# Kernel tuning notes

Measured on AMD Instinct MI355X. Metric: run time of the kernel, lower is better.

Reference implementation:

```python
import jax, jax.numpy as jnp
import numpy as np

B, S, D_MODEL, D_K, D_V = 8, 2048, 1024, 64, 64
NEG = -1e9


def setup_inputs() -> dict:
    key = jax.random.key(0)
    ks = jax.random.split(key, 12)
    inv = 1.0 / np.sqrt(D_MODEL)
    return {
        "q": jax.random.normal(ks[0], (B, S, D_MODEL), jnp.float32),
        "k": jax.random.normal(ks[1], (B, S, D_MODEL), jnp.float32),
        "v": jax.random.normal(ks[2], (B, S, D_MODEL), jnp.float32),
        "mask": jax.random.randint(ks[3], (1, S, S), 0, 2, jnp.int32),
        # Linear weights stored as [in, out] so y = x @ W + b
        "Wq": jax.random.normal(ks[4], (D_MODEL, D_K), jnp.float32) * inv,
        "bq": jnp.zeros((D_K,), jnp.float32),
        "Wk": jax.random.normal(ks[5], (D_MODEL, D_K), jnp.float32) * inv,
        "bk": jnp.zeros((D_K,), jnp.float32),
        "Wv": jax.random.normal(ks[6], (D_MODEL, D_V), jnp.float32) * inv,
        "bv": jnp.zeros((D_V,), jnp.float32),
        "Wo": jax.random.normal(ks[7], (D_V, D_MODEL), jnp.float32) * (1.0 / np.sqrt(D_V)),
        "bo": jnp.zeros((D_MODEL,), jnp.float32),
    }


def reference(q, k, v, mask, Wq, bq, Wk, bk, Wv, bv, Wo, bo):
    # single-head projections: [b, s, d_model] -> [b, s, d_k/d_v]
    qp = q @ Wq + bq
    kp = k @ Wk + bk
    vp = v @ Wv + bv
    # UNSCALED dot-product scores (original has no 1/sqrt(d_k)): [b, s, s]
    scores = jnp.einsum("bqd,bkd->bqk", qp, kp)
    scores = jnp.where(mask == 0, jnp.float32(NEG), scores)
    attn = jax.nn.softmax(scores, axis=-1)  # dropout p=0.0 -> identity
    out = jnp.einsum("bqk,bkv->bqv", attn, vp)
    return out @ Wo + bo
```

## Files before the change

### kernel.cpp

```cpp
#include <hip/hip_runtime.h>
#include <hip/hip_bf16.h>

typedef __bf16 bf16_t;
typedef __attribute__((ext_vector_type(8))) __bf16 bf16x8;
typedef __attribute__((ext_vector_type(4))) float f32x4;

#define MFMA16(a, b, c) __builtin_amdgcn_mfma_f32_16x16x32_bf16((a), (b), (c), 0, 0, 0)

#define NB 8
#define SS 2048
#define DM 1024
#define DK 64
#define NROW (NB * SS)
#define NSPLIT 4
#define SPLEN (SS / NSPLIT)

typedef __attribute__((address_space(1))) const unsigned int ga_u32;
typedef __attribute__((address_space(3))) unsigned int ls_u32;
#define GLOAD16(g, l) \
  __builtin_amdgcn_global_load_lds((ga_u32*)(g), (ls_u32*)(l), 16, 0, 0)

union U16x8 { unsigned short u[8]; uint4 q; };
union U16x4 { unsigned short u[4]; ushort4 v; };

__device__ inline void split_hl(float x, unsigned short& h, unsigned short& l) {
  bf16_t hb = (bf16_t)x;
  bf16_t lb = (bf16_t)(x - (float)hb);
  h = *(unsigned short*)&hb;
  l = *(unsigned short*)&lb;
}

__global__ __launch_bounds__(256) void maskpack_kernel(
    const int* __restrict__ mask, unsigned int* __restrict__ mbits) {
  int idx = blockIdx.x * 256 + threadIdx.x;
  int q = idx >> 6, w = idx & 63;
  const int4* src = (const int4*)(mask + (q << 11) + (w << 5));
  unsigned int bits = 0u;
#pragma unroll
  for (int i = 0; i < 8; ++i) {
    int4 t = src[i];
    bits |= (t.x != 0 ? 1u : 0u) << (i * 4 + 0);
    bits |= (t.y != 0 ? 1u : 0u) << (i * 4 + 1);
    bits |= (t.z != 0 ? 1u : 0u) << (i * 4 + 2);
    bits |= (t.w != 0 ? 1u : 0u) << (i * 4 + 3);
  }
  mbits[idx] = bits;
}

__global__ __launch_bounds__(256) void wprep_kernel(
    const float* __restrict__ Wq, const float* __restrict__ Wk,
    const float* __restrict__ Wv, char* __restrict__ wimg) {
  int which = blockIdx.x >> 6;
  const float* W = which == 0 ? Wq : (which == 1 ? Wk : Wv);
  char* img = wimg + (size_t)which * 16 * 16384;
  int e = (blockIdx.x & 63) * 256 + threadIdx.x;
  int k = e >> 4, n0 = (e & 15) << 2;
  float4 f = *(const float4*)(W + k * 64 + n0);
  float fv[4] = {f.x, f.y, f.z, f.w};
  char* base = img + (k >> 6) * 16384;
  int kk = k & 63;
#pragma unroll
  for (int u = 0; u < 4; ++u) {
    int n = n0 + u;
    unsigned short h, l;
    split_hl(fv[u], h, l);
    int byte = n * 128 + ((2 * kk) ^ ((n & 7) << 4));
    *(unsigned short*)(base + byte) = h;
    *(unsigned short*)(base + 8192 + byte) = l;
  }
}

__global__ __launch_bounds__(256) void proj3_kernel(
    const float* __restrict__ qx, const float* __restrict__ kx,
    const float* __restrict__ vx, const char* __restrict__ wimg,
    const float* __restrict__ bq, const float* __restrict__ bk,
    const float* __restrict__ bv, bf16_t* __restrict__ qhi,
    bf16_t* __restrict__ qlo, char* __restrict__ kimg,
    char* __restrict__ vimg) {
  __shared__ __align__(16) char smem[49664];
  char* xbuf = smem;
  char* wbuf = smem + 33280;
  const int mode = blockIdx.y;
  const float* X = mode == 0 ? qx : (mode == 1 ? kx : vx);
  const float* bias = mode == 0 ? bq : (mode == 1 ? bk : bv);
  const char* Xb = (const char*)X;
  const int tid = threadIdx.x;
  const int lane = tid & 63;
  const int wv = tid >> 6;
  const int lr = lane & 15;
  const int g = lane >> 4;
  const int wm = wv & 1;
  const int wn = wv >> 1;
  const int rbase = blockIdx.x * 32;
  const char* wsrc0 = wimg + (size_t)mode * 16 * 16384;

  f32x4 acc[2] = {};

  auto stageX = [&](int sc) {
#pragma unroll
    for (int j = 0; j < 8; ++j) {
      int u = wv * 8 + j;
      GLOAD16(Xb + (size_t)(rbase + u) * 4096 + sc * 1024 + lane * 16,
              xbuf + u * 1040 + lane * 16);
    }
  };
  auto stageW = [&](int idx) {
    const char* wsrc = wsrc0 + idx * 16384;
#pragma unroll
    for (int v = 0; v < 4; ++v)
      GLOAD16(wsrc + v * 4096 + tid * 16, wbuf + v * 4096 + tid * 16);
  };

  stageX(0);
  stageW(0);
  asm volatile("s_waitcnt vmcnt(0)" ::: "memory");
  __builtin_amdgcn_s_barrier();
  __builtin_amdgcn_sched_barrier(0);

  for (int idx = 0; idx < 16; ++idx) {
    {
      const int sub = idx & 3;
      const char* xrow = xbuf + (wm * 16 + lr) * 1040 + sub * 256;
#pragma unroll
      for (int ks = 0; ks < 2; ++ks) {
        float4 f0 = *(const float4*)(xrow + ks * 128 + g * 32);
        float4 f1 = *(const float4*)(xrow + ks * 128 + g * 32 + 16);
        float xv[8] = {f0.x, f0.y, f0.z, f0.w, f1.x, f1.y, f1.z, f1.w};
        bf16x8 ah, al;
#pragma unroll
        for (int i = 0; i < 8; ++i) {
          unsigned short h, l;
          split_hl(xv[i], h, l);
          ((unsigned short*)&ah)[i] = h;
          ((unsigned short*)&al)[i] = l;
        }
#pragma unroll
        for (int c = 0; c < 2; ++c) {
          int n = wn * 32 + c * 16 + lr;
          int swb = (n & 7) << 4;
          int co = ks * 64 + g * 16;
          bf16x8 bh = *(const bf16x8*)(wbuf + n * 128 + (co ^ swb));
          bf16x8 bl = *(const bf16x8*)(wbuf + 8192 + n * 128 + (co ^ swb));
          acc[c] = MFMA16(ah, bl, acc[c]);
          acc[c] = MFMA16(al, bh, acc[c]);
          acc[c] = MFMA16(ah, bh, acc[c]);
        }
      }
    }
    __builtin_amdgcn_sched_barrier(0);
    __builtin_amdgcn_s_barrier();
    if (idx < 15) {
      if ((idx & 3) == 3) stageX((idx >> 2) + 1);
      stageW(idx + 1);
      asm volatile("s_waitcnt vmcnt(0)" ::: "memory");
      __builtin_amdgcn_s_barrier();
      __builtin_amdgcn_sched_barrier(0);
    }
  }

  __syncthreads();
  float* sacc = (float*)smem;
#pragma unroll
  for (int c = 0; c < 2; ++c)
#pragma unroll
    for (int j = 0; j < 4; ++j)
      sacc[(wm * 16 + g * 4 + j) * 69 + wn * 32 + c * 16 + lr] = acc[c][j];
  __syncthreads();

  const int b = rbase >> 11;
  const int t = (rbase & (SS - 1)) >> 6;
  const int rt0 = rbase & 63;
  if (mode == 0) {
    int r = tid & 31, cg = tid >> 5;
    int row = rbase + r;
    U16x8 h, l;
#pragma unroll
    for (int i = 0; i < 8; ++i) {
      float v = sacc[r * 69 + cg * 8 + i] + bias[cg * 8 + i];
      split_hl(v, h.u[i], l.u[i]);
    }
    *(uint4*)((char*)qhi + (size_t)row * 128 + cg * 16) = h.q;
    *(uint4*)((char*)qlo + (size_t)row * 128 + cg * 16) = l.q;
  } else if (mode == 1) {
    int r = tid & 31, cg = tid >> 5;
    int rr = rt0 + r;
    char* base = kimg + (((size_t)(b * 32 + t)) << 14);
    int off = rr * 128 + ((cg * 16) ^ ((rr & 7) << 4));
    U16x8 h, l;
#pragma unroll
    for (int i = 0; i < 8; ++i) {
      float v = sacc[r * 69 + cg * 8 + i] + bias[cg * 8 + i];
      split_hl(v, h.u[i], l.u[i]);
    }
    *(uint4*)(base + off) = h.q;
    *(uint4*)(base + 8192 + off) = l.q;
  } else {
    int d = tid & 63, rg = tid >> 6;
    char* base = vimg + (((size_t)(b * 32 + t)) << 14);
    float bv = bias[d];
    U16x8 h, l;
#pragma unroll
    for (int i = 0; i < 8; ++i) {
      float v = sacc[(rg * 8 + i) * 69 + d] + bv;
      split_hl(v, h.u[i], l.u[i]);
    }
    int off = d * 128 + (((rt0 + rg * 8) * 2) ^ ((d & 7) << 4));
    *(uint4*)(base + off) = h.q;
    *(uint4*)(base + 8192 + off) = l.q;
  }
}

__global__ __launch_bounds__(256) void attn_kernel(
    const bf16_t* __restrict__ qhi, const bf16_t* __restrict__ qlo,
    const char* __restrict__ kimg, const char* __restrict__ vimg,
    const unsigned int* __restrict__ mbits, float* __restrict__ part_acc,
    float* __restrict__ part_m, float* __restrict__ part_l) {
  __shared__ __align__(16) char kbuf[16384];
  __shared__ __align__(16) char vbuf[16384];
  __shared__ __align__(16) char plds_all[4][2048];
  const int tid = threadIdx.x;
  const int lane = tid & 63;
  const int wv = tid >> 6;
  const int lr = lane & 15;
  const int g = lane >> 4;
  char* plds = &plds_all[wv][0];
  const int qrow0 = (blockIdx.x * 4 + wv) * 16;
  const int split = blockIdx.y;
  const int kv0 = split * SPLEN;
  const int b = qrow0 >> 11;
  const int sq0 = (qrow0 & (SS - 1)) + g * 4;

  const bf16_t* qh = qhi + (qrow0 + lr) * DK + g * 8;
  const bf16_t* ql = qlo + (qrow0 + lr) * DK + g * 8;
  bf16x8 qh0 = *(const bf16x8*)qh;
  bf16x8 qh1 = *(const bf16x8*)(qh + 32);
  bf16x8 ql0 = *(const bf16x8*)ql;
  bf16x8 ql1 = *(const bf16x8*)(ql + 32);

  float m[4], lsum[4];
  f32x4 acc[4] = {};
#pragma unroll
  for (int j = 0; j < 4; ++j) { m[j] = -3.0e38f; lsum[j] = 0.f; }

  for (int it = 0; it < SPLEN / 64; ++it) {
    const int tglob = (kv0 >> 6) + it;
    const char* ksrc = kimg + (((size_t)(b * 32 + tglob)) << 14);
    const char* vsrc = vimg + (((size_t)(b * 32 + tglob)) << 14);
#pragma unroll
    for (int u = 0; u < 4; ++u) {
      GLOAD16(ksrc + tid * 16 + u * 4096, kbuf + tid * 16 + u * 4096);
      GLOAD16(vsrc + tid * 16 + u * 4096, vbuf + tid * 16 + u * 4096);
    }
    asm volatile("s_waitcnt vmcnt(0)\n" ::: "memory");
    __syncthreads();
    f32x4 sac[4];
#pragma unroll
    for (int t = 0; t < 4; ++t) {
      int rk = t * 16 + lr;
      int sw = (rk & 7) << 4;
      bf16x8 kh0 = *(const bf16x8*)(kbuf + rk * 128 + ((g * 16) ^ sw));
      bf16x8 kh1 = *(const bf16x8*)(kbuf + rk * 128 + ((64 + g * 16) ^ sw));
      bf16x8 kl0 = *(const bf16x8*)(kbuf + 8192 + rk * 128 + ((g * 16) ^ sw));
      bf16x8 kl1 =
          *(const bf16x8*)(kbuf + 8192 + rk * 128 + ((64 + g * 16) ^ sw));
      f32x4 s = {};
      s = MFMA16(qh0, kl0, s);
      s = MFMA16(qh1, kl1, s);
      s = MFMA16(ql0, kh0, s);
      s = MFMA16(ql1, kh1, s);
      s = MFMA16(qh0, kh0, s);
      s = MFMA16(qh1, kh1, s);
      sac[t] = s;
    }
    const int wbase = (kv0 >> 5) + it * 2;
    uint2 m2[4];
#pragma unroll
    for (int j = 0; j < 4; ++j)
      m2[j] = *(const uint2*)(mbits + (sq0 + j) * 64 + wbase);
#pragma unroll
    for (int t = 0; t < 4; ++t)
#pragma unroll
      for (int j = 0; j < 4; ++j) {
        unsigned w = (t & 2) ? m2[j].y : m2[j].x;
        if (!((w >> ((t & 1) * 16 + lr)) & 1u)) sac[t][j] = -1e9f;
      }
#pragma unroll
    for (int j = 0; j < 4; ++j) {
      float v = sac[0][j];
#pragma unroll
      for (int t = 1; t < 4; ++t) v = fmaxf(v, sac[t][j]);
      v = fmaxf(v, __shfl_xor(v, 1, 64));
      v = fmaxf(v, __shfl_xor(v, 2, 64));
      v = fmaxf(v, __shfl_xor(v, 4, 64));
      v = fmaxf(v, __shfl_xor(v, 8, 64));
      float mn = fmaxf(m[j], v);
      float sc = __expf(m[j] - mn);
      m[j] = mn;
      lsum[j] *= sc;
#pragma unroll
      for (int c = 0; c < 4; ++c) acc[c][j] *= sc;
    }
    float ps[4] = {0.f, 0.f, 0.f, 0.f};
#pragma unroll
    for (int t = 0; t < 4; ++t)
#pragma unroll
      for (int j = 0; j < 4; ++j) {
        float p = __expf(sac[t][j] - m[j]);
        bf16_t pb = (bf16_t)p;
        ps[j] += (float)pb;
        int row = g * 4 + j;
        int byte = row * 128 + (((t * 16 + lr) * 2) ^ ((row & 7) << 4));
        *(bf16_t*)(plds + byte) = pb;
      }
#pragma unroll
    for (int j = 0; j < 4; ++j) {
      float s_ = ps[j];
      s_ += __shfl_xor(s_, 1, 64);
      s_ += __shfl_xor(s_, 2, 64);
      s_ += __shfl_xor(s_, 4, 64);
      s_ += __shfl_xor(s_, 8, 64);
      lsum[j] += s_;
    }
    asm volatile("s_waitcnt lgkmcnt(0)\n" ::: "memory");
#pragma unroll
    for (int kt = 0; kt < 2; ++kt) {
      int pbyte = lr * 128 + ((kt * 64 + g * 16) ^ ((lr & 7) << 4));
      bf16x8 pa = *(const bf16x8*)(plds + pbyte);
#pragma unroll
      for (int c = 0; c < 4; ++c) {
        int n = c * 16 + lr;
        int swv = (n & 7) << 4;
        bf16x8 vfh = *(const bf16x8*)(vbuf + n * 128 + ((kt * 64 + g * 16) ^ swv));
        bf16x8 vfl =
            *(const bf16x8*)(vbuf + 8192 + n * 128 + ((kt * 64 + g * 16) ^ swv));
        acc[c] = MFMA16(pa, vfh, acc[c]);
        acc[c] = MFMA16(pa, vfl, acc[c]);
      }
    }
    __syncthreads();
  }
#pragma unroll
  for (int c = 0; c < 4; ++c)
#pragma unroll
    for (int j = 0; j < 4; ++j)
      part_acc[((size_t)split * NROW + qrow0 + g * 4 + j) * DK + c * 16 + lr] =
          acc[c][j];
  if (lr == 0) {
#pragma unroll
    for (int j = 0; j < 4; ++j) {
      part_m[split * NROW + qrow0 + g * 4 + j] = m[j];
      part_l[split * NROW + qrow0 + g * 4 + j] = lsum[j];
    }
  }
}

__global__ __launch_bounds__(256) void combine_kernel(
    const float* __restrict__ pacc, const float* __restrict__ pm,
    const float* __restrict__ pl, float* __restrict__ attn_f) {
  int idx = blockIdx.x * 256 + threadIdx.x;
  int row = idx >> 6;
  float m0 = pm[row], m1 = pm[NROW + row];
  float m2 = pm[2 * NROW + row], m3 = pm[3 * NROW + row];
  float M = fmaxf(fmaxf(m0, m1), fmaxf(m2, m3));
  float w0 = __expf(m0 - M), w1 = __expf(m1 - M);
  float w2 = __expf(m2 - M), w3 = __expf(m3 - M);
  float l = w0 * pl[row] + w1 * pl[NROW + row] + w2 * pl[2 * NROW + row] +
            w3 * pl[3 * NROW + row];
  float a = w0 * pacc[idx] + w1 * pacc[(size_t)NROW * DK + idx] +
            w2 * pacc[2 * (size_t)NROW * DK + idx] +
            w3 * pacc[3 * (size_t)NROW * DK + idx];
  attn_f[idx] = a / l;
}

__global__ __launch_bounds__(256) void oproj_kernel(
    const float* __restrict__ attn, const float* __restrict__ Wo,
    const float* __restrict__ bo, float* __restrict__ out) {
  __shared__ __align__(16) bf16_t wt[256 * 64];
  const int tid = threadIdx.x;
  const int lane = tid & 63;
  const int wv = tid >> 6;
  const int lr = lane & 15;
  const int g = lane >> 4;
  const int rbase = blockIdx.x * 64 + wv * 16;
  const int c0 = blockIdx.y * 256;
  {
    const int k = tid >> 2;
    const int n0 = (tid & 3) << 6;
    const float4* src = (const float4*)(Wo + k * DM + c0 + n0);
#pragma unroll
    for (int i = 0; i < 16; ++i) {
      float4 f = src[i];
      float fv[4] = {f.x, f.y, f.z, f.w};
#pragma unroll
      for (int u = 0; u < 4; ++u) {
        int n = n0 + i * 4 + u;
        int byte = (n << 7) + (k << 1);
        byte ^= (n & 7) << 4;
        *(bf16_t*)((char*)wt + byte) = (bf16_t)fv[u];
      }
    }
  }
  __syncthreads();
  const float* ab = attn + (rbase + lr) * DK + g * 8;
  float4 x0 = *(const float4*)ab;
  float4 x1 = *(const float4*)(ab + 4);
  float4 y0 = *(const float4*)(ab + 32);
  float4 y1 = *(const float4*)(ab + 36);
  float xv[8] = {x0.x, x0.y, x0.z, x0.w, x1.x, x1.y, x1.z, x1.w};
  float yv[8] = {y0.x, y0.y, y0.z, y0.w, y1.x, y1.y, y1.z, y1.w};
  bf16x8 ah0, al0, ah1, al1;
#pragma unroll
  for (int i = 0; i < 8; ++i) {
    ah0[i] = (bf16_t)xv[i];
    al0[i] = (bf16_t)(xv[i] - (float)ah0[i]);
    ah1[i] = (bf16_t)yv[i];
    al1[i] = (bf16_t)(yv[i] - (float)ah1[i]);
  }
  f32x4 acc[16] = {};
#pragma unroll
  for (int c = 0; c < 16; ++c) {
    int n = c * 16 + lr;
    int byte0 = (n << 7) + ((g * 8) << 1);
    byte0 ^= (n & 7) << 4;
    int byte1 = (n << 7) + ((32 + g * 8) << 1);
    byte1 ^= (n & 7) << 4;
    bf16x8 b0 = *(const bf16x8*)((const char*)wt + byte0);
    bf16x8 b1 = *(const bf16x8*)((const char*)wt + byte1);
    acc[c] = MFMA16(ah0, b0, acc[c]);
    acc[c] = MFMA16(al0, b0, acc[c]);
    acc[c] = MFMA16(ah1, b1, acc[c]);
    acc[c] = MFMA16(al1, b1, acc[c]);
  }
#pragma unroll
  for (int c = 0; c < 16; ++c) {
    float bv = bo[c0 + c * 16 + lr];
#pragma unroll
    for (int j = 0; j < 4; ++j)
      out[(rbase + g * 4 + j) * DM + c0 + c * 16 + lr] = acc[c][j] + bv;
  }
}

extern "C" void kernel_launch(void* const* d_in, const int* in_sizes, int n_in,
                              void* d_out, int out_size, void* d_ws,
                              size_t ws_size, hipStream_t stream) {
  const float* q = (const float*)d_in[0];
  const float* k = (const float*)d_in[1];
  const float* v = (const float*)d_in[2];
  const int* mask = (const int*)d_in[3];
  const float* Wq = (const float*)d_in[4];
  const float* bq = (const float*)d_in[5];
  const float* Wk = (const float*)d_in[6];
  const float* bk = (const float*)d_in[7];
  const float* Wv = (const float*)d_in[8];
  const float* bv = (const float*)d_in[9];
  const float* Wo = (const float*)d_in[10];
  const float* bo = (const float*)d_in[11];
  float* out = (float*)d_out;

  bf16_t* qhi = (bf16_t*)d_ws;
  bf16_t* qlo = qhi + (size_t)NROW * DK;
  char* kimg = (char*)(qlo + (size_t)NROW * DK);
  char* vimg = kimg + ((size_t)NB * 32 << 14);
  char* wimg = vimg + ((size_t)NB * 32 << 14);
  float* part_acc = (float*)(wimg + (size_t)3 * 16 * 16384);
  float* part_m = part_acc + (size_t)NSPLIT * NROW * DK;
  float* part_l = part_m + (size_t)NSPLIT * NROW;
  float* attn_f = part_l + (size_t)NSPLIT * NROW;
  unsigned int* mbits = (unsigned int*)(attn_f + (size_t)NROW * DK);

  maskpack_kernel<<<dim3(SS * (SS / 32) / 256), dim3(256), 0, stream>>>(mask,
                                                                        mbits);
  wprep_kernel<<<dim3(192), dim3(256), 0, stream>>>(Wq, Wk, Wv, wimg);
  proj3_kernel<<<dim3(NROW / 32, 3), dim3(256), 0, stream>>>(
      q, k, v, wimg, bq, bk, bv, qhi, qlo, kimg, vimg);
  attn_kernel<<<dim3(NROW / 64, NSPLIT), dim3(256), 0, stream>>>(
      qhi, qlo, kimg, vimg, mbits, part_acc, part_m, part_l);
  combine_kernel<<<dim3(NROW * DK / 256), dim3(256), 0, stream>>>(
      part_acc, part_m, part_l, attn_f);
  oproj_kernel<<<dim3(NROW / 64, DM / 256), dim3(256), 0, stream>>>(attn_f, Wo,
                                                                    bo, out);
}
```

Before: 147.7 us.

## Double-buffer weight tiles and prefetch X through registers with split-once bf16 conversion

```diff
diff --git a/kernel.cpp b/kernel.cpp
--- a/kernel.cpp
+++ b/kernel.cpp
@@ -77,13 +77,11 @@
     const float* __restrict__ bv, bf16_t* __restrict__ qhi,
     bf16_t* __restrict__ qlo, char* __restrict__ kimg,
     char* __restrict__ vimg) {
-  __shared__ __align__(16) char smem[49664];
+  __shared__ __align__(16) char smem[40960];
   char* xbuf = smem;
-  char* wbuf = smem + 33280;
   const int mode = blockIdx.y;
   const float* X = mode == 0 ? qx : (mode == 1 ? kx : vx);
   const float* bias = mode == 0 ? bq : (mode == 1 ? bk : bv);
-  const char* Xb = (const char*)X;
   const int tid = threadIdx.x;
   const int lane = tid & 63;
   const int wv = tid >> 6;
@@ -92,72 +90,91 @@
   const int wm = wv & 1;
   const int wn = wv >> 1;
   const int rbase = blockIdx.x * 32;
+  const int xr = tid >> 3;
+  const int fo = (tid & 7) * 8;
+  const int row_local = wm * 16 + lr;
+  const int swa = (row_local & 7) << 4;
+  const int swx = (xr & 7) << 4;
+
+  f32x4 acc[2] = {};
   const char* wsrc0 = wimg + (size_t)mode * 16 * 16384;
 
-  f32x4 acc[2] = {};
-
-  auto stageX = [&](int sc) {
-#pragma unroll
-    for (int j = 0; j < 8; ++j) {
-      int u = wv * 8 + j;
-      GLOAD16(Xb + (size_t)(rbase + u) * 4096 + sc * 1024 + lane * 16,
-              xbuf + u * 1040 + lane * 16);
-    }
+  f32x4 xa, xb;
+  auto issueX = [&](int ch) {
+    const f32x4* xp =
+        (const f32x4*)(X + (size_t)(rbase + xr) * DM + ch * 64 + fo);
+    xa = xp[0];
+    xb = xp[1];
   };
-  auto stageW = [&](int idx) {
-    const char* wsrc = wsrc0 + idx * 16384;
-#pragma unroll
-    for (int v = 0; v < 4; ++v)
-      GLOAD16(wsrc + v * 4096 + tid * 16, wbuf + v * 4096 + tid * 16);
+  auto writeX = [&]() {
+    float xv[8] = {xa[0], xa[1], xa[2], xa[3], xb[0], xb[1], xb[2], xb[3]};
+    U16x8 hq, lq;
+#pragma unroll
+    for (int i = 0; i < 8; ++i) split_hl(xv[i], hq.u[i], lq.u[i]);
+    char* xh = xbuf + xr * 128;
+    int b0 = 2 * fo;
+    *(uint4*)(xh + (b0 ^ swx)) = hq.q;
+    *(uint4*)(xh + 4096 + (b0 ^ swx)) = lq.q;
   };
-
-  stageX(0);
-  stageW(0);
-  asm volatile("s_waitcnt vmcnt(0)" ::: "memory");
+  auto stageW = [&](int ch, char* dst) {
+    const char* wsrc = wsrc0 + ch * 16384;
+#pragma unroll
+    for (int u = 0; u < 4; ++u)
+      GLOAD16(wsrc + u * 4096 + tid * 16, dst + u * 4096 + tid * 16);
+  };
+  auto compute = [&](const char* wb) {
+#pragma unroll
+    for (int ks = 0; ks < 2; ++ks) {
+      int co = ks * 64 + g * 16;
+      bf16x8 ah = *(const bf16x8*)(xbuf + row_local * 128 + (co ^ swa));
+      bf16x8 al = *(const bf16x8*)(xbuf + 4096 + row_local * 128 + (co ^ swa));
+#pragma unroll
+      for (int c = 0; c < 2; ++c) {
+        int n = wn * 32 + c * 16 + lr;
+        int swb = (n & 7) << 4;
+        bf16x8 bh = *(const bf16x8*)(wb + n * 128 + (co ^ swb));
+        bf16x8 bl = *(const bf16x8*)(wb + 8192 + n * 128 + (co ^ swb));
+        acc[c] = MFMA16(ah, bl, acc[c]);
+        acc[c] = MFMA16(al, bh, acc[c]);
+        acc[c] = MFMA16(ah, bh, acc[c]);
+      }
+    }
+  };
+
+  issueX(0);
+  __builtin_amdgcn_sched_barrier(0);
+  stageW(0, smem + 8192);
+  __builtin_amdgcn_sched_barrier(0);
+  writeX();
+  issueX(1);
+  __builtin_amdgcn_sched_barrier(0);
+  asm volatile("s_waitcnt vmcnt(2)" ::: "memory");
+  asm volatile("s_waitcnt lgkmcnt(0)" ::: "memory");
   __builtin_amdgcn_s_barrier();
   __builtin_amdgcn_sched_barrier(0);
 
-  for (int idx = 0; idx < 16; ++idx) {
-    {
-      const int sub = idx & 3;
-      const char* xrow = xbuf + (wm * 16 + lr) * 1040 + sub * 256;
-#pragma unroll
-      for (int ks = 0; ks < 2; ++ks) {
-        float4 f0 = *(const float4*)(xrow + ks * 128 + g * 32);
-        float4 f1 = *(const float4*)(xrow + ks * 128 + g * 32 + 16);
-        float xv[8] = {f0.x, f0.y, f0.z, f0.w, f1.x, f1.y, f1.z, f1.w};
-        bf16x8 ah, al;
-#pragma unroll
-        for (int i = 0; i < 8; ++i) {
-          unsigned short h, l;
-          split_hl(xv[i], h, l);
-          ((unsigned short*)&ah)[i] = h;
-          ((unsigned short*)&al)[i] = l;
-        }
-#pragma unroll
-        for (int c = 0; c < 2; ++c) {
-          int n = wn * 32 + c * 16 + lr;
-          int swb = (n & 7) << 4;
-          int co = ks * 64 + g * 16;
-          bf16x8 bh = *(const bf16x8*)(wbuf + n * 128 + (co ^ swb));
-          bf16x8 bl = *(const bf16x8*)(wbuf + 8192 + n * 128 + (co ^ swb));
-          acc[c] = MFMA16(ah, bl, acc[c]);
-          acc[c] = MFMA16(al, bh, acc[c]);
-          acc[c] = MFMA16(ah, bh, acc[c]);
-        }
-      }
-    }
-    __builtin_amdgcn_sched_barrier(0);
-    __builtin_amdgcn_s_barrier();
-    if (idx < 15) {
-      if ((idx & 3) == 3) stageX((idx >> 2) + 1);
-      stageW(idx + 1);
-      asm volatile("s_waitcnt vmcnt(0)" ::: "memory");
+  for (int ch = 0; ch < 16; ++ch) {
+    char* wc = (ch & 1) ? smem + 24576 : smem + 8192;
+    char* wn_ = (ch & 1) ? smem + 8192 : smem + 24576;
+    if (ch < 15) stageW(ch + 1, wn_);
+    compute(wc);
+    if (ch < 15) {
+      __builtin_amdgcn_sched_barrier(0);
       __builtin_amdgcn_s_barrier();
       __builtin_amdgcn_sched_barrier(0);
-    }
-  }
-
+      writeX();
+      if (ch < 14) {
+        issueX(ch + 2);
+        __builtin_amdgcn_sched_barrier(0);
+        asm volatile("s_waitcnt vmcnt(2)" ::: "memory");
+      } else {
+        asm volatile("s_waitcnt vmcnt(0)" ::: "memory");
+      }
+      asm volatile("s_waitcnt lgkmcnt(0)" ::: "memory");
+      __builtin_amdgcn_s_barrier();
+      __builtin_amdgcn_sched_barrier(0);
+    }
+  }
   __syncthreads();
   float* sacc = (float*)smem;
 #pragma unroll
```

Result: no change. 150.6 us (+2.0%).
